# Optimization experiments

Hardware: AMD Instinct MI355X
Metric: run time of the kernel (lower is better)

The kernel has to match this reference:

```python
import jax, jax.numpy as jnp
import numpy as np

H, W = 32, 32
C = 512
HEADS = 8
HEAD_DIM = C // HEADS
B = 8
GROUPS = 32
EPS = 1e-6
N = H * W


def _rel_indices():
    # (N, N) lookup indices into the (2H-1)*(2W-1) relative-position table
    y = np.arange(H)
    x = np.arange(W)
    y1, x1, y2, x2 = np.meshgrid(y, x, y, x, indexing='ij')
    idx = (y1 - y2 + H - 1) * (2 * W - 1) + (x1 - x2 + W - 1)
    return jnp.asarray(idx.reshape(N, N), dtype=jnp.int32)

REL_IDX = _rel_indices()


def setup_inputs() -> dict:
    key = jax.random.key(0)
    ks = jax.random.split(key, 8)
    s = 0.02
    return {
        'x': jax.random.normal(ks[0], (B, C, H, W), jnp.float32),
        '_1': jnp.zeros((1,), jnp.int32),
        '_2': jnp.zeros((1,), jnp.int32),
        'gamma': jnp.ones((C,), jnp.float32),
        'beta': jnp.zeros((C,), jnp.float32),
        'wq': jax.random.normal(ks[1], (C, C), jnp.float32) * s,
        'bq': jnp.zeros((C,), jnp.float32),
        'wk': jax.random.normal(ks[2], (C, C), jnp.float32) * s,
        'bk': jnp.zeros((C,), jnp.float32),
        'wv': jax.random.normal(ks[3], (C, C), jnp.float32) * s,
        'bv': jnp.zeros((C,), jnp.float32),
        'wproj': jax.random.normal(ks[4], (C, C), jnp.float32) * s,
        'bproj': jnp.zeros((C,), jnp.float32),
        'pos_enc': jax.random.normal(ks[5], (HEADS, (2 * H - 1) * (2 * W - 1)), jnp.float32) * s,
    }


def _group_norm(x, gamma, beta):
    b, c, h, w = x.shape
    xg = x.reshape(b, GROUPS, c // GROUPS, h, w)
    mean = xg.mean(axis=(2, 3, 4), keepdims=True)
    var = xg.var(axis=(2, 3, 4), keepdims=True)
    xg = (xg - mean) * jax.lax.rsqrt(var + EPS)
    x = xg.reshape(b, c, h, w)
    return x * gamma[None, :, None, None] + beta[None, :, None, None]


def reference(x, _1, _2, gamma, beta, wq, bq, wk, bk, wv, bv, wproj, bproj, pos_enc):
    x0 = x
    xn = _group_norm(x, gamma, beta)
    xt = xn.reshape(B, C, N)  # (B, C, N)

    def proj(w, bias):
        # 1x1 conv == channel matmul: (B, C_out, N)
        y = jnp.einsum('oc,bcn->bon', w, xt) + bias[None, :, None]
        # split heads: channel index = head*HEAD_DIM + d -> (B, heads, N, d)
        return y.reshape(B, HEADS, HEAD_DIM, N).transpose(0, 1, 3, 2)

    q = proj(wq, bq)
    k = proj(wk, bk)
    v = proj(wv, bv)

    scale = 1.0 / jnp.sqrt(jnp.float32(HEAD_DIM))
    attn = jnp.einsum('bhqd,bhkd->bhqk', q, k) * scale  # (B, heads, N, N)
    rel_bias = pos_enc[:, REL_IDX]  # (heads, N, N)
    attn = attn + rel_bias[None]
    attn = jax.nn.softmax(attn, axis=-1)

    out = jnp.einsum('bhqk,bhkd->bhqd', attn, v)  # (B, heads, N, d)
    out = out.transpose(0, 1, 3, 2).reshape(B, C, H, W)
    out = jnp.einsum('oc,bchw->bohw', wproj, out) + bproj[None, :, None, None]
    return out + x0
```

## Files before the change

kernel.cpp:

```cpp
#include <hip/hip_runtime.h>
#include <hip/hip_bf16.h>
#include <math.h>

typedef __bf16 bf16_t;
typedef __bf16 bf16x8 __attribute__((ext_vector_type(8)));
typedef __bf16 bf16x4 __attribute__((ext_vector_type(4)));
typedef float  f32x4  __attribute__((ext_vector_type(4)));

#define MFMA16(a, b, c) __builtin_amdgcn_mfma_f32_16x16x32_bf16((a), (b), (c), 0, 0, 0)
#define GLDS16(g, s) __builtin_amdgcn_global_load_lds( \
    (const __attribute__((address_space(1))) void*)(g), \
    (__attribute__((address_space(3))) void*)(s), 16, 0, 0)

#define LOG2E 1.4426950408889634f

__global__ __launch_bounds__(256) void cast_weights(
    const float* __restrict__ wq, const float* __restrict__ wk,
    const float* __restrict__ wv, const float* __restrict__ wp,
    bf16_t* __restrict__ Wqkv, bf16_t* __restrict__ Wp)
{
    const int i = (blockIdx.x * 256 + threadIdx.x) * 4;
#pragma unroll
    for (int j = 0; j < 4; ++j) {
        Wqkv[i + j]          = (bf16_t)wq[i + j];
        Wqkv[262144 + i + j] = (bf16_t)wk[i + j];
        Wqkv[524288 + i + j] = (bf16_t)wv[i + j];
        Wp[i + j]            = (bf16_t)wp[i + j];
    }
}

__global__ __launch_bounds__(256) void bias_kernel(
    const float* __restrict__ pos, bf16_t* __restrict__ Bias2)
{
    const int h   = blockIdx.x >> 6;
    const int qt  = blockIdx.x & 63;
    const int qy  = qt >> 1;
    const int qxb = (qt & 1) * 16;
    const int t = threadIdx.x;
    __shared__ bf16_t ps[32][64];

    for (int i = t; i < 32 * 63; i += 256) {
        const int r = i / 63, dx = i - r * 63;
        ps[r][dx] = (bf16_t)(pos[h * 3969 + (qy + r) * 63 + dx] * LOG2E);
    }
    __syncthreads();

    bf16_t* outb = Bias2 + (((size_t)h * 64 + qt) * 64) * 256;
#pragma unroll
    for (int it = 0; it < 16; ++it) {
        const int idx = t + it * 256;
        const int kt = idx >> 6, l = idx & 63;
        const int qx  = qxb + (l & 15);
        const int nk0 = kt * 16 + (l >> 4) * 4;
        const int ky = nk0 >> 5;
        const int kx0 = nk0 & 31;
        const int r = 31 - ky;
        const int dx0 = qx - kx0 + 31;
        bf16x4 o;
#pragma unroll
        for (int j = 0; j < 4; ++j) o[j] = ps[r][dx0 - j];
        *(bf16x4*)(outb + (size_t)idx * 4) = o;
    }
}

__global__ __launch_bounds__(512) void gn_kernel(
    const float* __restrict__ x, const float* __restrict__ gamma,
    const float* __restrict__ beta, bf16_t* __restrict__ xnT)
{
    const int blk = blockIdx.x;
    const int b = blk >> 5, g = blk & 31;
    const int t = threadIdx.x;
    const int hi = t >> 8, tl = t & 255;
    __shared__ float red[16];
    const float* base = x + ((size_t)b * 512 + g * 16) * 1024;

    f32x4 v[8];
    float s = 0.f, s2 = 0.f;
#pragma unroll
    for (int it = 0; it < 8; ++it) {
        v[it] = *(const f32x4*)(base + (size_t)hi * 8192 + it * 1024 + tl * 4);
#pragma unroll
        for (int j = 0; j < 4; ++j) { s += v[it][j]; s2 += v[it][j] * v[it][j]; }
    }
#pragma unroll
    for (int m = 1; m < 64; m <<= 1) { s += __shfl_xor(s, m); s2 += __shfl_xor(s2, m); }
    const int w = t >> 6;
    if ((t & 63) == 0) { red[w] = s; red[8 + w] = s2; }
    __syncthreads();
    s = 0.f; s2 = 0.f;
#pragma unroll
    for (int i = 0; i < 8; ++i) { s += red[i]; s2 += red[8 + i]; }
    const float mean = s * (1.f / 16384.f);
    const float var  = fmaxf(s2 * (1.f / 16384.f) - mean * mean, 0.f);
    const float rstd = rsqrtf(var + 1e-6f);

    float ga[8], be[8];
#pragma unroll
    for (int it = 0; it < 8; ++it) {
        const int gc = g * 16 + hi * 8 + it;
        ga[it] = gamma[gc] * rstd;
        be[it] = beta[gc] - mean * ga[it];
    }
#pragma unroll
    for (int j = 0; j < 4; ++j) {
        bf16x8 o;
#pragma unroll
        for (int it = 0; it < 8; ++it)
            o[it] = (bf16_t)(v[it][j] * ga[it] + be[it]);
        *(bf16x8*)(xnT + ((size_t)b * 1024 + tl * 4 + j) * 512 + g * 16 + hi * 8) = o;
    }
}

__global__ __launch_bounds__(256) void gemm_bt(
    const bf16_t* __restrict__ A, const bf16_t* __restrict__ Bt, int mode,
    int mtiles,
    const float* __restrict__ bias0, const float* __restrict__ bias1,
    const float* __restrict__ bias2,
    const float* __restrict__ x0, float* __restrict__ outF,
    bf16_t* __restrict__ Qb, bf16_t* __restrict__ Kb, bf16_t* __restrict__ Vb)
{
    const int K  = 512;
    const int g  = blockIdx.x;
    const int xcd = g & 7;
    const int i_  = g >> 3;
    const int m_idx = i_ % mtiles;
    const int n_idx = xcd * 8 + i_ / mtiles;
    const int m0 = m_idx * 128;
    const int n0 = n_idx * 128;
    const int t = threadIdx.x;
    const int l = t & 63, w = t >> 6;
    const int wr = w >> 1, wc = w & 1;
    const int lrow = l & 15, lgrp = l >> 4;

    __shared__ __align__(16) char smem_raw[128 * 136 * 2];
    bf16_t* AsF = (bf16_t*)smem_raw;
    bf16_t* BsF = AsF + 8192;
    bf16_t* Ct  = (bf16_t*)smem_raw;

    f32x4 acc[4][4];
#pragma unroll
    for (int i = 0; i < 4; ++i)
#pragma unroll
        for (int j = 0; j < 4; ++j) acc[i][j] = (f32x4){0.f, 0.f, 0.f, 0.f};

    const bf16_t* gA0 = A  + (size_t)(m0 + w * 16 + (l >> 2)) * K + (l & 3) * 8;
    const bf16_t* gA1 = gA0 + (size_t)64 * K;
    const bf16_t* gB0 = Bt + (size_t)(n0 + w * 16 + (l >> 2)) * K + (l & 3) * 8;
    const bf16_t* gB1 = gB0 + (size_t)64 * K;

    GLDS16(gA0, &AsF[w * 512]);
    GLDS16(gA1, &AsF[2048 + w * 512]);
    GLDS16(gB0, &BsF[w * 512]);
    GLDS16(gB1, &BsF[2048 + w * 512]);
    __syncthreads();

    int cur = 0;
    for (int tk = 0; tk < 16; ++tk) {
        if (tk < 15) {
            const int k0 = (tk + 1) * 32;
            const int nb = cur ^ 1;
            GLDS16(gA0 + k0, &AsF[nb * 4096 + w * 512]);
            GLDS16(gA1 + k0, &AsF[nb * 4096 + 2048 + w * 512]);
            GLDS16(gB0 + k0, &BsF[nb * 4096 + w * 512]);
            GLDS16(gB1 + k0, &BsF[nb * 4096 + 2048 + w * 512]);
        }
        const bf16_t* Asb = AsF + cur * 4096;
        const bf16_t* Bsb = BsF + cur * 4096;
        bf16x8 af[4], bfr[4];
#pragma unroll
        for (int ms = 0; ms < 4; ++ms)
            af[ms] = *(const bf16x8*)&Asb[(wr * 64 + ms * 16 + lrow) * 32 + lgrp * 8];
#pragma unroll
        for (int ns = 0; ns < 4; ++ns)
            bfr[ns] = *(const bf16x8*)&Bsb[(wc * 64 + ns * 16 + lrow) * 32 + lgrp * 8];
#pragma unroll
        for (int ms = 0; ms < 4; ++ms)
#pragma unroll
            for (int ns = 0; ns < 4; ++ns)
                acc[ms][ns] = MFMA16(af[ms], bfr[ns], acc[ms][ns]);
        if (tk < 15) __syncthreads();
        cur ^= 1;
    }

    if (mode == 0) {
        const int which = m0 >> 9;
        const int mq = (m0 >> 7) & 3;
        const float* bias = (which == 0) ? bias0 : (which == 1) ? bias1 : bias2;
        const float scl = (which == 0) ? 0.125f * LOG2E : 1.0f;
        const int b   = n_idx >> 3;
        const int nn0 = (n_idx & 7) * 128;

        __syncthreads();
        if (which < 2) {
            bf16_t* Qk = (which == 0) ? Qb : Kb;
#pragma unroll
            for (int ms = 0; ms < 4; ++ms) {
                const int ml = wr * 64 + ms * 16 + lgrp * 4;
#pragma unroll
                for (int ns = 0; ns < 4; ++ns) {
                    const int nl = wc * 64 + ns * 16 + lrow;
                    bf16x4 pk;
#pragma unroll
                    for (int j = 0; j < 4; ++j)
                        pk[j] = (bf16_t)((acc[ms][ns][j] + bias[mq * 128 + ml + j]) * scl);
                    *(bf16x4*)&Ct[nl * 136 + ml] = pk;
                }
            }
            __syncthreads();
#pragma unroll
            for (int it = 0; it < 8; ++it) {
                const int idx = it * 256 + t;
                const int token = idx >> 4, oc = idx & 15;
                const bf16x8 vv8 = *(const bf16x8*)&Ct[token * 136 + oc * 8];
                const int head = mq * 2 + (oc >> 3);
                const int d = (oc & 7) * 8;
                *(bf16x8*)(Qk + (((size_t)b * 8 + head) * 1024 + nn0 + token) * 64 + d) = vv8;
            }
        } else {
#pragma unroll
            for (int ms = 0; ms < 4; ++ms) {
                const int ml = wr * 64 + ms * 16 + lgrp * 4;
#pragma unroll
                for (int ns = 0; ns < 4; ++ns) {
                    const int nl = wc * 64 + ns * 16 + lrow;
#pragma unroll
                    for (int j = 0; j < 4; ++j)
                        Ct[(ml + j) * 136 + nl] =
                            (bf16_t)(acc[ms][ns][j] + bias[mq * 128 + ml + j]);
                }
            }
            __syncthreads();
#pragma unroll
            for (int it = 0; it < 8; ++it) {
                const int idx = it * 256 + t;
                const int o = idx >> 4, nc = idx & 15;
                const bf16x8 vv8 = *(const bf16x8*)&Ct[o * 136 + nc * 8];
                const int head = mq * 2 + (o >> 6);
                const int d = o & 63;
                *(bf16x8*)(Vb + (((size_t)b * 8 + head) * 64 + d) * 1024 + nn0 + nc * 8) = vv8;
            }
        }
    } else {
#pragma unroll
        for (int ms = 0; ms < 4; ++ms) {
#pragma unroll
            for (int ns = 0; ns < 4; ++ns) {
                const int c  = m0 + wr * 64 + ms * 16 + lgrp * 4;
                const int np = n0 + wc * 64 + ns * 16 + lrow;
                const int b = np >> 10, n = np & 1023;
#pragma unroll
                for (int j = 0; j < 4; ++j) {
                    const size_t idx = ((size_t)b * 512 + c + j) * 1024 + n;
                    outF[idx] = acc[ms][ns][j] + bias0[c + j] + x0[idx];
                }
            }
        }
    }
}

__global__ __launch_bounds__(512) void attn_kernel(
    const bf16_t* __restrict__ Qb, const bf16_t* __restrict__ Kb,
    const bf16_t* __restrict__ Vb, const bf16_t* __restrict__ Bias2,
    bf16_t* __restrict__ Xo)
{
    const int bh = blockIdx.x;
    const int h  = bh & 7;
    const int q0 = blockIdx.y * 128;
    const int t = threadIdx.x;
    const int w = t >> 6, l = t & 63;
    const int lrow = l & 15, lgrp = l >> 4;

    __shared__ __align__(16) bf16_t Ks[64][72];
    __shared__ __align__(16) bf16_t Vs[64][72];
    __shared__ __align__(16) bf16_t Ps[8][16][72];

    const int qrow = q0 + w * 16 + lrow;
    const bf16_t* qbase = Qb + ((size_t)bh * 1024 + qrow) * 64;
    const bf16x8 qf0 = *(const bf16x8*)(qbase + lgrp * 8);
    const bf16x8 qf1 = *(const bf16x8*)(qbase + 32 + lgrp * 8);

    const bf16_t* bb = Bias2 + (((size_t)h * 64 + (q0 >> 4) + w) * 64) * 256;

    float ts = 0.f;
    f32x4 oacc[4];
#pragma unroll
    for (int j = 0; j < 4; ++j) oacc[j] = (f32x4){0.f, 0.f, 0.f, 0.f};

    const int sr2 = t >> 3;
    const int sc2 = (t & 7) * 8;
    const bf16_t* Kg = Kb + ((size_t)bh * 1024 + sr2) * 64 + sc2;
    const bf16_t* Vg = Vb + ((size_t)bh * 64 + sr2) * 1024 + sc2;

    bf16x8 kv = *(const bf16x8*)(Kg);
    bf16x8 vv = *(const bf16x8*)(Vg);
    bf16x4 bA[4], bB[4];
#pragma unroll
    for (int ns = 0; ns < 4; ++ns)
        bA[ns] = *(const bf16x4*)(bb + (size_t)(ns * 64 + l) * 4);

    auto tile = [&](int tt, bf16x4 (&bcur)[4], bf16x4 (&bnxt)[4]) {
        const int nk0 = tt * 64;
        __syncthreads();
        *(bf16x8*)&Ks[sr2][sc2] = kv;
        *(bf16x8*)&Vs[sr2][sc2] = vv;
        __syncthreads();
        if (tt < 15) {
            const int nkn = nk0 + 64;
#pragma unroll
            for (int ns = 0; ns < 4; ++ns)
                bnxt[ns] = *(const bf16x4*)(bb + (size_t)(((nkn >> 4) + ns) * 64 + l) * 4);
            kv = *(const bf16x8*)(Kg + (size_t)nkn * 64);
            vv = *(const bf16x8*)(Vg + nkn);
        }

        f32x4 s[4];
#pragma unroll
        for (int ns = 0; ns < 4; ++ns) {
            f32x4 z = (f32x4){(float)bcur[ns][0], (float)bcur[ns][1],
                              (float)bcur[ns][2], (float)bcur[ns][3]};
            const bf16x8 kf0 = *(const bf16x8*)&Ks[ns * 16 + lrow][lgrp * 8];
            const bf16x8 kf1 = *(const bf16x8*)&Ks[ns * 16 + lrow][32 + lgrp * 8];
            z = MFMA16(kf0, qf0, z);
            z = MFMA16(kf1, qf1, z);
            s[ns] = z;
        }
#pragma unroll
        for (int ns = 0; ns < 4; ++ns) {
            float p0 = exp2f(s[ns][0]), p1 = exp2f(s[ns][1]);
            float p2 = exp2f(s[ns][2]), p3 = exp2f(s[ns][3]);
            ts += (p0 + p1) + (p2 + p3);
            bf16x4 pk;
            pk[0] = (bf16_t)p0; pk[1] = (bf16_t)p1;
            pk[2] = (bf16_t)p2; pk[3] = (bf16_t)p3;
            *(bf16x4*)&Ps[w][lrow][ns * 16 + lgrp * 4] = pk;
        }
        const bf16x8 pf0 = *(const bf16x8*)&Ps[w][lrow][lgrp * 8];
        const bf16x8 pf1 = *(const bf16x8*)&Ps[w][lrow][32 + lgrp * 8];
#pragma unroll
        for (int ds = 0; ds < 4; ++ds) {
            const bf16x8 vf0 = *(const bf16x8*)&Vs[ds * 16 + lrow][lgrp * 8];
            const bf16x8 vf1 = *(const bf16x8*)&Vs[ds * 16 + lrow][32 + lgrp * 8];
            oacc[ds] = MFMA16(vf0, pf0, oacc[ds]);
            oacc[ds] = MFMA16(vf1, pf1, oacc[ds]);
        }
    };

    for (int t2 = 0; t2 < 16; t2 += 2) {
        tile(t2,     bA, bB);
        tile(t2 + 1, bB, bA);
    }

    ts += __shfl_xor(ts, 16);
    ts += __shfl_xor(ts, 32);
    const float inv = 1.0f / ts;

    const int b = bh >> 3;
    const int q = q0 + w * 16 + lrow;
    bf16_t* xrow = Xo + ((size_t)b * 1024 + q) * 512 + h * 64;
#pragma unroll
    for (int ds = 0; ds < 4; ++ds) {
        bf16x4 o4;
#pragma unroll
        for (int j = 0; j < 4; ++j) o4[j] = (bf16_t)(oacc[ds][j] * inv);
        *(bf16x4*)(xrow + ds * 16 + lgrp * 4) = o4;
    }
}

extern "C" void kernel_launch(void* const* d_in, const int* in_sizes, int n_in,
                              void* d_out, int out_size, void* d_ws, size_t ws_size,
                              hipStream_t stream)
{
    const float* x     = (const float*)d_in[0];
    const float* gamma = (const float*)d_in[3];
    const float* beta  = (const float*)d_in[4];
    const float* wq    = (const float*)d_in[5];
    const float* bq    = (const float*)d_in[6];
    const float* wk    = (const float*)d_in[7];
    const float* bk    = (const float*)d_in[8];
    const float* wv    = (const float*)d_in[9];
    const float* bv    = (const float*)d_in[10];
    const float* wp    = (const float*)d_in[11];
    const float* bp    = (const float*)d_in[12];
    const float* pos   = (const float*)d_in[13];
    float* out = (float*)d_out;

    size_t off = 0;
    char* wsb = (char*)d_ws;
    auto alloc = [&](size_t bytes) { char* p = wsb + off; off += bytes; return p; };
    bf16_t* Wqkv  = (bf16_t*)alloc((size_t)1536 * 512 * 2);
    bf16_t* Wp    = (bf16_t*)alloc((size_t)512 * 512 * 2);
    bf16_t* xnT   = (bf16_t*)alloc((size_t)8192 * 512 * 2);
    bf16_t* Qb    = (bf16_t*)alloc((size_t)8192 * 512 * 2);
    bf16_t* Kb    = (bf16_t*)alloc((size_t)8192 * 512 * 2);
    bf16_t* Vb    = (bf16_t*)alloc((size_t)8192 * 512 * 2);
    bf16_t* Xo    = (bf16_t*)alloc((size_t)8192 * 512 * 2);
    bf16_t* Bias2 = (bf16_t*)alloc((size_t)8 * 64 * 64 * 64 * 4 * 2);

    hipLaunchKernelGGL(cast_weights, dim3(256), dim3(256), 0, stream,
                       wq, wk, wv, wp, Wqkv, Wp);
    hipLaunchKernelGGL(bias_kernel, dim3(512), dim3(256), 0, stream, pos, Bias2);
    hipLaunchKernelGGL(gn_kernel, dim3(256), dim3(512), 0, stream,
                       x, gamma, beta, xnT);
    hipLaunchKernelGGL(gemm_bt, dim3(768), dim3(256), 0, stream,
                       Wqkv, xnT, 0, 12, bq, bk, bv,
                       nullptr, nullptr, Qb, Kb, Vb);
    hipLaunchKernelGGL(attn_kernel, dim3(64, 8), dim3(512), 0, stream,
                       Qb, Kb, Vb, Bias2, Xo);
    hipLaunchKernelGGL(gemm_bt, dim3(256), dim3(256), 0, stream,
                       Wp, Xo, 1, 4, bp, nullptr, nullptr,
                       x, out, nullptr, nullptr, nullptr);
}
```

Baseline: 99.05 us.

## Double attention KV tile to 128 keys and compute row sums via MFMA

The attention kernel now stages 128 keys of K and V per synchronization step instead of 64, halving the number of barrier pairs and deepening the prefetch of K, V and bias. It also replaces the scalar exp-sum accumulation and its cross-lane shuffles with an extra MFMA against a ones vector, so the softmax denominator comes out of the matrix unit. The cost is larger LDS usage and more registers for the prefetched data, which may reduce occupancy. The row sums are also now taken from the bf16-rounded probabilities rather than the fp32 values.

```diff
diff --git a/kernel.cpp b/kernel.cpp
--- a/kernel.cpp
+++ b/kernel.cpp
@@ -270,8 +270,8 @@
     const int w = t >> 6, l = t & 63;
     const int lrow = l & 15, lgrp = l >> 4;
 
-    __shared__ __align__(16) bf16_t Ks[64][72];
-    __shared__ __align__(16) bf16_t Vs[64][72];
+    __shared__ __align__(16) bf16_t Ks[128][72];
+    __shared__ __align__(16) bf16_t Vs[64][136];
     __shared__ __align__(16) bf16_t Ps[8][16][72];
 
     const int qrow = q0 + w * 16 + lrow;
@@ -281,8 +281,11 @@
 
     const bf16_t* bb = Bias2 + (((size_t)h * 64 + (q0 >> 4) + w) * 64) * 256;
 
-    float ts = 0.f;
-    f32x4 oacc[4];
+    bf16x8 ones;
+#pragma unroll
+    for (int i = 0; i < 8; ++i) ones[i] = (bf16_t)1.0f;
+
+    f32x4 oacc[4], tsacc = (f32x4){0.f, 0.f, 0.f, 0.f};
 #pragma unroll
     for (int j = 0; j < 4; ++j) oacc[j] = (f32x4){0.f, 0.f, 0.f, 0.f};
 
@@ -291,68 +294,77 @@
     const bf16_t* Kg = Kb + ((size_t)bh * 1024 + sr2) * 64 + sc2;
     const bf16_t* Vg = Vb + ((size_t)bh * 64 + sr2) * 1024 + sc2;
 
-    bf16x8 kv = *(const bf16x8*)(Kg);
-    bf16x8 vv = *(const bf16x8*)(Vg);
-    bf16x4 bA[4], bB[4];
-#pragma unroll
-    for (int ns = 0; ns < 4; ++ns)
-        bA[ns] = *(const bf16x4*)(bb + (size_t)(ns * 64 + l) * 4);
-
-    auto tile = [&](int tt, bf16x4 (&bcur)[4], bf16x4 (&bnxt)[4]) {
-        const int nk0 = tt * 64;
+    bf16x8 kv0 = *(const bf16x8*)(Kg);
+    bf16x8 kv1 = *(const bf16x8*)(Kg + (size_t)64 * 64);
+    bf16x8 vv0 = *(const bf16x8*)(Vg);
+    bf16x8 vv1 = *(const bf16x8*)(Vg + 64);
+    bf16x4 bA[8], bB[8];
+#pragma unroll
+    for (int k = 0; k < 8; ++k)
+        bA[k] = *(const bf16x4*)(bb + (size_t)(k * 64 + l) * 4);
+
+    auto dtile = [&](int it, bf16x4 (&bcur)[8], bf16x4 (&bnxt)[8]) {
+        const int nk0 = it * 128;
         __syncthreads();
-        *(bf16x8*)&Ks[sr2][sc2] = kv;
-        *(bf16x8*)&Vs[sr2][sc2] = vv;
+        *(bf16x8*)&Ks[sr2][sc2]      = kv0;
+        *(bf16x8*)&Ks[64 + sr2][sc2] = kv1;
+        *(bf16x8*)&Vs[sr2][sc2]      = vv0;
+        *(bf16x8*)&Vs[sr2][64 + sc2] = vv1;
         __syncthreads();
-        if (tt < 15) {
-            const int nkn = nk0 + 64;
-#pragma unroll
-            for (int ns = 0; ns < 4; ++ns)
-                bnxt[ns] = *(const bf16x4*)(bb + (size_t)(((nkn >> 4) + ns) * 64 + l) * 4);
-            kv = *(const bf16x8*)(Kg + (size_t)nkn * 64);
-            vv = *(const bf16x8*)(Vg + nkn);
+        if (it < 7) {
+            const int nkn = nk0 + 128;
+#pragma unroll
+            for (int k = 0; k < 8; ++k)
+                bnxt[k] = *(const bf16x4*)(bb + (size_t)((((nkn >> 4)) + k) * 64 + l) * 4);
+            kv0 = *(const bf16x8*)(Kg + (size_t)nkn * 64);
+            kv1 = *(const bf16x8*)(Kg + (size_t)(nkn + 64) * 64);
+            vv0 = *(const bf16x8*)(Vg + nkn);
+            vv1 = *(const bf16x8*)(Vg + nkn + 64);
         }
 
-        f32x4 s[4];
-#pragma unroll
-        for (int ns = 0; ns < 4; ++ns) {
-            f32x4 z = (f32x4){(float)bcur[ns][0], (float)bcur[ns][1],
-                              (float)bcur[ns][2], (float)bcur[ns][3]};
-            const bf16x8 kf0 = *(const bf16x8*)&Ks[ns * 16 + lrow][lgrp * 8];
-            const bf16x8 kf1 = *(const bf16x8*)&Ks[ns * 16 + lrow][32 + lgrp * 8];
-            z = MFMA16(kf0, qf0, z);
-            z = MFMA16(kf1, qf1, z);
-            s[ns] = z;
-        }
-#pragma unroll
-        for (int ns = 0; ns < 4; ++ns) {
-            float p0 = exp2f(s[ns][0]), p1 = exp2f(s[ns][1]);
-            float p2 = exp2f(s[ns][2]), p3 = exp2f(s[ns][3]);
-            ts += (p0 + p1) + (p2 + p3);
-            bf16x4 pk;
-            pk[0] = (bf16_t)p0; pk[1] = (bf16_t)p1;
-            pk[2] = (bf16_t)p2; pk[3] = (bf16_t)p3;
-            *(bf16x4*)&Ps[w][lrow][ns * 16 + lgrp * 4] = pk;
-        }
-        const bf16x8 pf0 = *(const bf16x8*)&Ps[w][lrow][lgrp * 8];
-        const bf16x8 pf1 = *(const bf16x8*)&Ps[w][lrow][32 + lgrp * 8];
-#pragma unroll
-        for (int ds = 0; ds < 4; ++ds) {
-            const bf16x8 vf0 = *(const bf16x8*)&Vs[ds * 16 + lrow][lgrp * 8];
-            const bf16x8 vf1 = *(const bf16x8*)&Vs[ds * 16 + lrow][32 + lgrp * 8];
-            oacc[ds] = MFMA16(vf0, pf0, oacc[ds]);
-            oacc[ds] = MFMA16(vf1, pf1, oacc[ds]);
+#pragma unroll
+        for (int st = 0; st < 2; ++st) {
+            f32x4 s[4];
+#pragma unroll
+            for (int ns = 0; ns < 4; ++ns) {
+                const bf16x4 bc = bcur[st * 4 + ns];
+                f32x4 z = (f32x4){(float)bc[0], (float)bc[1],
+                                  (float)bc[2], (float)bc[3]};
+                const bf16x8 kf0 = *(const bf16x8*)&Ks[st * 64 + ns * 16 + lrow][lgrp * 8];
+                const bf16x8 kf1 = *(const bf16x8*)&Ks[st * 64 + ns * 16 + lrow][32 + lgrp * 8];
+                z = MFMA16(kf0, qf0, z);
+                z = MFMA16(kf1, qf1, z);
+                s[ns] = z;
+            }
+#pragma unroll
+            for (int ns = 0; ns < 4; ++ns) {
+                bf16x4 pk;
+                pk[0] = (bf16_t)exp2f(s[ns][0]);
+                pk[1] = (bf16_t)exp2f(s[ns][1]);
+                pk[2] = (bf16_t)exp2f(s[ns][2]);
+                pk[3] = (bf16_t)exp2f(s[ns][3]);
+                *(bf16x4*)&Ps[w][lrow][ns * 16 + lgrp * 4] = pk;
+            }
+            const bf16x8 pf0 = *(const bf16x8*)&Ps[w][lrow][lgrp * 8];
+            const bf16x8 pf1 = *(const bf16x8*)&Ps[w][lrow][32 + lgrp * 8];
+            tsacc = MFMA16(ones, pf0, tsacc);
+            tsacc = MFMA16(ones, pf1, tsacc);
+#pragma unroll
+            for (int ds = 0; ds < 4; ++ds) {
+                const bf16x8 vf0 = *(const bf16x8*)&Vs[ds * 16 + lrow][st * 64 + lgrp * 8];
+                const bf16x8 vf1 = *(const bf16x8*)&Vs[ds * 16 + lrow][st * 64 + 32 + lgrp * 8];
+                oacc[ds] = MFMA16(vf0, pf0, oacc[ds]);
+                oacc[ds] = MFMA16(vf1, pf1, oacc[ds]);
+            }
         }
     };
 
-    for (int t2 = 0; t2 < 16; t2 += 2) {
-        tile(t2,     bA, bB);
-        tile(t2 + 1, bB, bA);
-    }
-
-    ts += __shfl_xor(ts, 16);
-    ts += __shfl_xor(ts, 32);
-    const float inv = 1.0f / ts;
+    for (int it2 = 0; it2 < 8; it2 += 2) {
+        dtile(it2,     bA, bB);
+        dtile(it2 + 1, bB, bA);
+    }
+
+    const float inv = 1.0f / tsacc[0];
 
     const int b = bh >> 3;
     const int q = q0 + w * 16 + lrow;
```

New measurement: 97.27 us. About the same (-1.8%).
